# Kernel tuning notes

Measured on AMD Instinct MI355X. Metric: run time of the kernel, lower is better.

Reference implementation:

```python
import jax, jax.numpy as jnp
import numpy as np

D_MODEL = 1024
N_HEADS = 16
HEAD_DIM = D_MODEL // N_HEADS
NEG_INF = -1e9


def setup_inputs() -> dict:
    key = jax.random.key(0)
    ks = jax.random.split(key, 12)
    B, S = 2, 2048
    std = 1.0 / np.sqrt(D_MODEL)
    def lin(k):
        kw, kb = jax.random.split(k)
        W = jax.random.uniform(kw, (D_MODEL, D_MODEL), jnp.float32, -std, std)
        b = jax.random.uniform(kb, (D_MODEL,), jnp.float32, -std, std)
        return W, b
    Wq, bq = lin(ks[0])
    Wk, bk = lin(ks[1])
    Wv, bv = lin(ks[2])
    Wo, bo = lin(ks[3])
    Q = jax.random.normal(ks[4], (B, S, D_MODEL), jnp.float32)
    K = jax.random.normal(ks[5], (B, S, D_MODEL), jnp.float32)
    V = jax.random.normal(ks[6], (B, S, D_MODEL), jnp.float32)
    # causal attention mask: True means masked (disallowed)
    attn_mask = jnp.triu(jnp.ones((S, S), dtype=bool), k=1)
    padding_mask = jnp.zeros((B, S), dtype=bool)  # no padding
    return {"Q": Q, "K": K, "V": V, "attn_mask": attn_mask,
            "padding_mask": padding_mask,
            "Wq": Wq, "bq": bq, "Wk": Wk, "bk": bk,
            "Wv": Wv, "bv": bv, "Wo": Wo, "bo": bo}


def reference(Q, K, V, attn_mask, padding_mask, Wq, bq, Wk, bk, Wv, bv, Wo, bo):
    B, Sq, _ = Q.shape
    Sk = K.shape[1]
    # QKV projections, split into heads -> [B, H, S, Dh]
    def proj(x, W, b):
        y = x @ W.T + b
        return y.reshape(B, -1, N_HEADS, HEAD_DIM).transpose(0, 2, 1, 3)
    q = proj(Q, Wq, bq)
    k = proj(K, Wk, bk)
    v = proj(V, Wv, bv)
    # scaled dot-product attention (dropout is identity in eval mode)
    scores = jnp.einsum('bhqd,bhkd->bhqk', q, k) / jnp.sqrt(
        jnp.asarray(HEAD_DIM, q.dtype))
    mask = attn_mask[None, None, :, :] | padding_mask[:, None, None, :]
    scores = jnp.where(mask, NEG_INF, scores)
    attn = jax.nn.softmax(scores, axis=-1)
    x = jnp.einsum('bhqk,bhkd->bhqd', attn, v)
    x = x.transpose(0, 2, 1, 3).reshape(B, Sq, D_MODEL)
    return x @ Wo.T + bo
```

## Files before the change

kernel.cpp:

```cpp
#include <hip/hip_runtime.h>
#include <hip/hip_bf16.h>
#include <cstddef>
#include <cstdint>

#define S_LEN  2048
#define DMODEL 1024
#define NHEADS 16

typedef __attribute__((ext_vector_type(8))) short  short8;
typedef __attribute__((ext_vector_type(4))) short  s16x4;
typedef __attribute__((ext_vector_type(8))) __bf16 bf16x8;
typedef __attribute__((ext_vector_type(4))) float  f32x4;

__device__ __forceinline__ f32x4 MFMA(short8 a, short8 b, f32x4 c) {
    return __builtin_amdgcn_mfma_f32_16x16x32_bf16(
        __builtin_bit_cast(bf16x8, a), __builtin_bit_cast(bf16x8, b), c, 0, 0, 0);
}

__device__ __forceinline__ unsigned short f2bs(float f) {
    return __builtin_bit_cast(unsigned short, __float2bfloat16(f));
}
__device__ __forceinline__ float bs2f(unsigned short u) {
    unsigned int x = ((unsigned int)u) << 16;
    return __builtin_bit_cast(float, x);
}

__device__ __forceinline__ short8 cvt8(f32x4 a, f32x4 b) {
    short8 r;
#pragma unroll
    for (int i = 0; i < 4; ++i) {
        r[i]     = (short)f2bs(a[i]);
        r[4 + i] = (short)f2bs(b[i]);
    }
    return r;
}

__device__ __forceinline__ short8 scale8(short8 v) {
    short8 r;
#pragma unroll
    for (int i = 0; i < 8; ++i)
        r[i] = (short)f2bs(bs2f((unsigned short)v[i]) * 0.125f);
    return r;
}

__device__ __forceinline__ int xcd_swz(int bid, int nwg) {
    const int chunk = nwg >> 3;
    return (bid & 7) * chunk + (bid >> 3);
}

__device__ __forceinline__ void bar_sync() {
    asm volatile("s_waitcnt lgkmcnt(0)" ::: "memory");
    __builtin_amdgcn_sched_barrier(0);
    __builtin_amdgcn_s_barrier();
}

#define GLDS16(src, dst) __builtin_amdgcn_global_load_lds( \
    (__attribute__((address_space(1))) void*)(src),        \
    (__attribute__((address_space(3))) void*)(dst), 16, 0, 0)

struct FS { f32x4 v[2][2]; };

__global__ __launch_bounds__(256)
void wcvt(const float* __restrict__ Wq, const float* __restrict__ Wk,
          const float* __restrict__ Wv, unsigned short* __restrict__ wb)
{
    const int i = blockIdx.x * 256 + threadIdx.x;
    const float* src = (i < 131072) ? Wq : (i < 262144) ? Wk : Wv;
    const size_t j = (size_t)(i & 131071) * 8;
    const short8 v = cvt8(((const f32x4*)(src + j))[0], ((const f32x4*)(src + j))[1]);
    *(short8*)(wb + (size_t)i * 8) = v;
}

__global__ __launch_bounds__(256, 3)
void qkv_gemm(const float* __restrict__ Q, const float* __restrict__ K,
              const float* __restrict__ V,
              const unsigned short* __restrict__ wb,
              const float* __restrict__ bq, const float* __restrict__ bk,
              const float* __restrict__ bv,
              unsigned short* qh, unsigned short* kh, unsigned short* vh)
{
    __shared__ short a_lds[2][128 * 32];
    __shared__ short w_lds[2][128 * 32];

    const int swz = xcd_swz(blockIdx.x, 768);
    const int z   = swz >> 8;
    const int rem = swz & 255;
    const int m0  = (rem >> 3) * 128;
    const int n0  = (rem & 7) * 128;

    const float *A, *B_; unsigned short* O;
    if (z == 0)      { A = Q; B_ = bq; O = qh; }
    else if (z == 1) { A = K; B_ = bk; O = kh; }
    else             { A = V; B_ = bv; O = vh; }
    const unsigned short* W = wb + ((size_t)z << 20);

    const int t    = threadIdx.x;
    const int lane = t & 63;
    const int wid  = t >> 6;
    const int wr   = (wid >> 1) << 6;
    const int wc   = (wid & 1) << 6;
    const int fr   = lane & 15;
    const int ks   = lane >> 4;

    const int row0 = t >> 2,         sl0 = t & 3;
    const int row1 = (256 + t) >> 2, sl1 = (256 + t) & 3;
    const int ms0  = sl0 ^ ((row0 >> 1) & 3);
    const int ms1  = sl1 ^ ((row1 >> 1) & 3);

    const int g0 = wid * 2, g1 = g0 + 1;
    const int gsl   = lane & 3;
    const int grow0 = g0 * 16 + (lane >> 2);
    const int grow1 = g1 * 16 + (lane >> 2);
    const int ssl0  = gsl ^ ((grow0 >> 1) & 3);
    const int ssl1  = gsl ^ ((grow1 >> 1) & 3);

    auto load_R = [&](FS& S, int k0) {
        const float* p0 = A + (size_t)(m0 + row0) * DMODEL + k0 + sl0 * 8;
        S.v[0][0] = ((const f32x4*)p0)[0]; S.v[0][1] = ((const f32x4*)p0)[1];
        const float* p1 = A + (size_t)(m0 + row1) * DMODEL + k0 + sl1 * 8;
        S.v[1][0] = ((const f32x4*)p1)[0]; S.v[1][1] = ((const f32x4*)p1)[1];
    };
    auto store_R = [&](const FS& S, int buf) {
        *(short8*)&a_lds[buf][row0 * 32 + ms0 * 8] = cvt8(S.v[0][0], S.v[0][1]);
        *(short8*)&a_lds[buf][row1 * 32 + ms1 * 8] = cvt8(S.v[1][0], S.v[1][1]);
    };
    auto gload_G = [&](int k0, int buf) {
        GLDS16(W + (size_t)(n0 + grow0) * DMODEL + k0 + ssl0 * 8, &w_lds[buf][g0 * 512]);
        GLDS16(W + (size_t)(n0 + grow1) * DMODEL + k0 + ssl1 * 8, &w_lds[buf][g1 * 512]);
    };

    f32x4 acc[4][4] = {};
    auto compute = [&](int cur) {
        short8 af[4], bfr[4];
#pragma unroll
        for (int i = 0; i < 4; ++i) {
            const int ra = wr + i * 16 + fr;
            af[i]  = *(const short8*)&a_lds[cur][ra * 32 + ((ks ^ ((ra >> 1) & 3)) << 3)];
            const int rb = wc + i * 16 + fr;
            bfr[i] = *(const short8*)&w_lds[cur][rb * 32 + ((ks ^ ((rb >> 1) & 3)) << 3)];
        }
#pragma unroll
        for (int mi = 0; mi < 4; ++mi)
#pragma unroll
            for (int ni = 0; ni < 4; ++ni)
                acc[mi][ni] = MFMA(af[mi], bfr[ni], acc[mi][ni]);
    };

    FS SA, SB;
    gload_G(0, 0);
    load_R(SA, 0);
    store_R(SA, 0);
    load_R(SB, 32);
    bar_sync();

    for (int tt = 0; tt < 30; tt += 2) {
        gload_G((tt + 1) * 32, 1);
        load_R(SA, (tt + 2) * 32);
        compute(0);
        store_R(SB, 1);
        asm volatile("s_waitcnt vmcnt(4)" ::: "memory");
        bar_sync();
        gload_G((tt + 2) * 32, 0);
        load_R(SB, (tt + 3) * 32);
        compute(1);
        store_R(SA, 0);
        asm volatile("s_waitcnt vmcnt(4)" ::: "memory");
        bar_sync();
    }
    gload_G(31 * 32, 1);
    compute(0);
    store_R(SB, 1);
    asm volatile("s_waitcnt vmcnt(0)" ::: "memory");
    bar_sync();
    compute(1);

#pragma unroll
    for (int ni = 0; ni < 4; ++ni) {
        const int n    = n0 + wc + ni * 16 + fr;
        const float bv = B_[n];
#pragma unroll
        for (int mi = 0; mi < 4; ++mi) {
#pragma unroll
            for (int j = 0; j < 4; ++j) {
                const int m = m0 + wr + mi * 16 + ks * 4 + j;
                const int b = m >> 11, s = m & (S_LEN - 1);
                const int hh = n >> 6, dh = n & 63;
                O[((((size_t)b * NHEADS + hh) * S_LEN + s) << 6) + dh]
                    = f2bs(acc[mi][ni][j] + bv);
            }
        }
    }
}

__global__ __launch_bounds__(256, 3)
void out_gemm(const unsigned short* __restrict__ X, const float* __restrict__ Wo,
              const float* __restrict__ bo, float* __restrict__ out)
{
    __shared__ short a_lds[2][128 * 32];
    __shared__ short w_lds[2][128 * 32];
    const int swz = xcd_swz(blockIdx.x, 256);
    const int m0  = (swz >> 3) * 128;
    const int n0  = (swz & 7) * 128;

    const int t    = threadIdx.x;
    const int lane = t & 63;
    const int wid  = t >> 6;
    const int wr   = (wid >> 1) << 6;
    const int wc   = (wid & 1) << 6;
    const int fr   = lane & 15;
    const int ks   = lane >> 4;

    const int row0 = t >> 2,         sl0 = t & 3;
    const int row1 = (256 + t) >> 2, sl1 = (256 + t) & 3;
    const int ms0  = sl0 ^ ((row0 >> 1) & 3);
    const int ms1  = sl1 ^ ((row1 >> 1) & 3);

    short8 av_b[2];
    f32x4  wv_f[2][2];

    auto load_tile = [&](int k0) {
        av_b[0] = *(const short8*)(X + (size_t)(m0 + row0) * DMODEL + k0 + sl0 * 8);
        av_b[1] = *(const short8*)(X + (size_t)(m0 + row1) * DMODEL + k0 + sl1 * 8);
        const float* pw0 = Wo + (size_t)(n0 + row0) * DMODEL + k0 + sl0 * 8;
        wv_f[0][0] = ((const f32x4*)pw0)[0]; wv_f[0][1] = ((const f32x4*)pw0)[1];
        const float* pw1 = Wo + (size_t)(n0 + row1) * DMODEL + k0 + sl1 * 8;
        wv_f[1][0] = ((const f32x4*)pw1)[0]; wv_f[1][1] = ((const f32x4*)pw1)[1];
    };
    auto store_tile = [&](int buf) {
        *(short8*)&a_lds[buf][row0 * 32 + ms0 * 8] = av_b[0];
        *(short8*)&a_lds[buf][row1 * 32 + ms1 * 8] = av_b[1];
        *(short8*)&w_lds[buf][row0 * 32 + ms0 * 8] = cvt8(wv_f[0][0], wv_f[0][1]);
        *(short8*)&w_lds[buf][row1 * 32 + ms1 * 8] = cvt8(wv_f[1][0], wv_f[1][1]);
    };

    load_tile(0);
    store_tile(0);
    load_tile(32);
    __syncthreads();

    f32x4 acc[4][4] = {};

    for (int kidx = 0; kidx < 32; ++kidx) {
        const int cur = kidx & 1;
        short8 af[4], bfr[4];
#pragma unroll
        for (int i = 0; i < 4; ++i) {
            const int ra = wr + i * 16 + fr;
            af[i]  = *(const short8*)&a_lds[cur][ra * 32 + ((ks ^ ((ra >> 1) & 3)) << 3)];
            const int rb = wc + i * 16 + fr;
            bfr[i] = *(const short8*)&w_lds[cur][rb * 32 + ((ks ^ ((rb >> 1) & 3)) << 3)];
        }
#pragma unroll
        for (int mi = 0; mi < 4; ++mi)
#pragma unroll
            for (int ni = 0; ni < 4; ++ni)
                acc[mi][ni] = MFMA(af[mi], bfr[ni], acc[mi][ni]);

        if (kidx + 1 < 32) {
            store_tile(cur ^ 1);
            if (kidx + 2 < 32) load_tile((kidx + 2) * 32);
        }
        __syncthreads();
    }

#pragma unroll
    for (int ni = 0; ni < 4; ++ni) {
        const int n    = n0 + wc + ni * 16 + fr;
        const float bv = bo[n];
#pragma unroll
        for (int mi = 0; mi < 4; ++mi)
#pragma unroll
            for (int j = 0; j < 4; ++j) {
                const int m = m0 + wr + mi * 16 + ks * 4 + j;
                out[(size_t)m * DMODEL + n] = acc[mi][ni][j] + bv;
            }
    }
}

#define VSTR 72
#define PSTR 88

struct QState {
    short8 qf0, qf1;
    f32x4  oacc[4];
    float  m, l;
    int    qr0;
};

__device__ __forceinline__ void attn_tile(QState& st, const int k0,
                                          const short* k_lds, const short* v_lds,
                                          short* p_buf, const int fr, const int ks)
{
    const int myq = st.qr0 + fr;
    f32x4 sacc[4] = {};
    __builtin_amdgcn_s_setprio(1);
#pragma unroll
    for (int nk = 0; nk < 4; ++nk) {
        const int rb = nk * 16 + fr;
        short8 a0 = *(const short8*)&k_lds[rb * 64 + (((ks)     ^ (rb & 7)) << 3)];
        short8 a1 = *(const short8*)&k_lds[rb * 64 + (((4 + ks) ^ (rb & 7)) << 3)];
        sacc[nk] = MFMA(a0, st.qf0, sacc[nk]);
        sacc[nk] = MFMA(a1, st.qf1, sacc[nk]);
    }
    __builtin_amdgcn_s_setprio(0);

    float mx = -1e9f;
    if (k0 + 63 <= st.qr0) {
#pragma unroll
        for (int nk = 0; nk < 4; ++nk)
#pragma unroll
            for (int jj = 0; jj < 4; ++jj) mx = fmaxf(mx, sacc[nk][jj]);
    } else {
#pragma unroll
        for (int nk = 0; nk < 4; ++nk)
#pragma unroll
            for (int jj = 0; jj < 4; ++jj) {
                const int key = k0 + nk * 16 + ks * 4 + jj;
                float s = (key <= myq) ? sacc[nk][jj] : -1e9f;
                sacc[nk][jj] = s;
                mx = fmaxf(mx, s);
            }
    }
    mx = fmaxf(mx, __shfl_xor(mx, 16));
    mx = fmaxf(mx, __shfl_xor(mx, 32));
    if (!__all(mx <= st.m + 8.f)) {
        const float mnew = fmaxf(st.m, mx);
        const float corr = __expf(st.m - mnew);
        st.m = mnew;
        st.l *= corr;
#pragma unroll
        for (int nd = 0; nd < 4; ++nd)
#pragma unroll
            for (int jj = 0; jj < 4; ++jj) st.oacc[nd][jj] *= corr;
    }

    float rsum = 0.f;
#pragma unroll
    for (int nk = 0; nk < 4; ++nk) {
        s16x4 pw;
#pragma unroll
        for (int jj = 0; jj < 4; ++jj) {
            const float p = __expf(sacc[nk][jj] - st.m);
            rsum += p;
            pw[jj] = (short)f2bs(p);
        }
        *(s16x4*)&p_buf[fr * PSTR + nk * 16 + ks * 4] = pw;
    }
    rsum += __shfl_xor(rsum, 16);
    rsum += __shfl_xor(rsum, 32);
    st.l += rsum;
    asm volatile("" ::: "memory");

    __builtin_amdgcn_s_setprio(1);
#pragma unroll
    for (int sh = 0; sh < 2; ++sh) {
        short8 pa = *(const short8*)&p_buf[fr * PSTR + sh * 32 + ks * 8];
#pragma unroll
        for (int nd = 0; nd < 4; ++nd) {
            short8 vf = *(const short8*)&v_lds[(nd * 16 + fr) * VSTR + sh * 32 + ks * 8];
            st.oacc[nd] = MFMA(vf, pa, st.oacc[nd]);
        }
    }
    __builtin_amdgcn_s_setprio(0);
}

__global__ __launch_bounds__(256, 2)
void attn_kernel(const unsigned short* __restrict__ qh,
                 const unsigned short* __restrict__ kh,
                 const unsigned short* __restrict__ vh,
                 unsigned short* __restrict__ xh)
{
    __shared__ short k_lds[64 * 64];
    __shared__ short v_lds[64 * VSTR];
    __shared__ short p_lds[4][16 * PSTR];

    const int t    = threadIdx.x;
    const int lane = t & 63;
    const int wid  = t >> 6;
    const int fr   = lane & 15;
    const int ks   = lane >> 4;
    const int swz  = xcd_swz(blockIdx.x, 512);
    const int bh   = swz >> 4;
    const int xp   = swz & 15;
    const int qa0  = xp * 64;
    const int qb0  = (31 - xp) * 64;
    const int ntA  = xp + 1;
    const int ntB  = 32 - xp;

    const unsigned short* qb_ = qh + ((size_t)bh << 17);
    const unsigned short* kb  = kh + ((size_t)bh << 17);
    const unsigned short* vb  = vh + ((size_t)bh << 17);

    QState A, B;
    A.qr0 = qa0 + wid * 16;  B.qr0 = qb0 + wid * 16;
    A.qf0 = scale8(*(const short8*)&qb_[(A.qr0 + fr) * 64 + ks * 8]);
    A.qf1 = scale8(*(const short8*)&qb_[(A.qr0 + fr) * 64 + 32 + ks * 8]);
    B.qf0 = scale8(*(const short8*)&qb_[(B.qr0 + fr) * 64 + ks * 8]);
    B.qf1 = scale8(*(const short8*)&qb_[(B.qr0 + fr) * 64 + 32 + ks * 8]);
#pragma unroll
    for (int nd = 0; nd < 4; ++nd) { A.oacc[nd] = f32x4{}; B.oacc[nd] = f32x4{}; }
    A.m = B.m = -1e9f; A.l = B.l = 0.f;

    short8 kv[2], vv[2];
#pragma unroll
    for (int cc = 0; cc < 2; ++cc) {
        const int c   = cc * 256 + t;
        const int row = c >> 3;
        const int sl  = c & 7;
        kv[cc] = *(const short8*)(kb + (size_t)row * 64 + sl * 8);
        const int key = c & 63;
        const int d0  = (c >> 6) * 8;
        vv[cc] = *(const short8*)(vb + (size_t)key * 64 + d0);
    }

    for (int kt = 0; kt < ntB; ++kt) {
        const int k0 = kt * 64;
        __syncthreads();

#pragma unroll
        for (int cc = 0; cc < 2; ++cc) {
            const int c   = cc * 256 + t;
            const int row = c >> 3;
            const int ms  = (c & 7) ^ (row & 7);
            *(short8*)&k_lds[row * 64 + ms * 8] = kv[cc];
            const int key = c & 63;
            const int d0  = (c >> 6) * 8;
#pragma unroll
            for (int i = 0; i < 8; ++i)
                v_lds[(d0 + i) * VSTR + key] = vv[cc][i];
        }
        __syncthreads();

        if (kt + 1 < ntB) {
            const int k1 = k0 + 64;
#pragma unroll
            for (int cc = 0; cc < 2; ++cc) {
                const int c   = cc * 256 + t;
                const int row = c >> 3;
                const int sl  = c & 7;
                kv[cc] = *(const short8*)(kb + (size_t)(k1 + row) * 64 + sl * 8);
                const int key = c & 63;
                const int d0  = (c >> 6) * 8;
                vv[cc] = *(const short8*)(vb + (size_t)(k1 + key) * 64 + d0);
            }
        }

        attn_tile(B, k0, k_lds, v_lds, p_lds[wid], fr, ks);
        if (kt < ntA)
            attn_tile(A, k0, k_lds, v_lds, p_lds[wid], fr, ks);
    }

    const int b = bh >> 4, h = bh & 15;
#pragma unroll
    for (int which = 0; which < 2; ++which) {
        QState& st = which ? B : A;
        const float inv = 1.f / st.l;
        const size_t base = ((size_t)b * S_LEN + (st.qr0 + fr)) * DMODEL + h * 64;
#pragma unroll
        for (int nd = 0; nd < 4; ++nd)
#pragma unroll
            for (int jj = 0; jj < 4; ++jj)
                xh[base + nd * 16 + ks * 4 + jj] = f2bs(st.oacc[nd][jj] * inv);
    }
}

extern "C" void kernel_launch(void* const* d_in, const int* in_sizes, int n_in,
                              void* d_out, int out_size, void* d_ws, size_t ws_size,
                              hipStream_t stream)
{
    const float* Q  = (const float*)d_in[0];
    const float* K  = (const float*)d_in[1];
    const float* V  = (const float*)d_in[2];
    const float* Wq = (const float*)d_in[5];
    const float* bq = (const float*)d_in[6];
    const float* Wk = (const float*)d_in[7];
    const float* bk = (const float*)d_in[8];
    const float* Wv = (const float*)d_in[9];
    const float* bv = (const float*)d_in[10];
    const float* Wo = (const float*)d_in[11];
    const float* bo = (const float*)d_in[12];
    float* out = (float*)d_out;

    const size_t HSZ = (size_t)2 * S_LEN * DMODEL;
    unsigned short* qh = (unsigned short*)d_ws;
    unsigned short* kh = qh + HSZ;
    unsigned short* vh = kh + HSZ;
    unsigned short* xh = vh + HSZ;
    unsigned short* wb = xh;

    wcvt<<<1536, 256, 0, stream>>>(Wq, Wk, Wv, wb);
    qkv_gemm<<<768, 256, 0, stream>>>(Q, K, V, wb, bq, bk, bv, qh, kh, vh);
    attn_kernel<<<512, 256, 0, stream>>>(qh, kh, vh, xh);
    out_gemm<<<256, 256, 0, stream>>>(xh, Wo, bo, out);
}
```

Baseline: 109.1 us.

## Pre-convert activations and weights to bf16, use async LDS-load GEMMs

Adds a single conversion kernel that turns Q, K, V and all four weight matrices into bf16 in workspace. New QKV and output GEMM kernels then stream these bf16 operands straight into LDS with global_load_lds through a triple-buffered, swizzled pipeline. This is meant to remove the in-GEMM fp32 loads and conversions and halve the bytes each GEMM tile reads. The cost is an extra full pass over the activations plus a much larger workspace, and the old path stays as a fallback when the workspace is too small.

```diff
diff --git a/kernel.cpp b/kernel.cpp
--- a/kernel.cpp
+++ b/kernel.cpp
@@ -6,6 +6,8 @@
 #define S_LEN  2048
 #define DMODEL 1024
 #define NHEADS 16
+#define ELT    1048576
+#define HSZe   (4 * ELT)
 
 typedef __attribute__((ext_vector_type(8))) short  short8;
 typedef __attribute__((ext_vector_type(4))) short  s16x4;
@@ -59,6 +61,140 @@
     (__attribute__((address_space(3))) void*)(dst), 16, 0, 0)
 
 struct FS { f32x4 v[2][2]; };
+
+__global__ __launch_bounds__(256)
+void xcvt(const float* __restrict__ Q, const float* __restrict__ K,
+          const float* __restrict__ V,
+          const float* __restrict__ Wq, const float* __restrict__ Wk,
+          const float* __restrict__ Wv, const float* __restrict__ Wo,
+          unsigned short* __restrict__ dst)
+{
+    const int gid = blockIdx.x * 256 + threadIdx.x;
+    const size_t e0 = (size_t)gid * 8;
+    const int seg = (int)(e0 >> 20);
+    const float* src; size_t off;
+    if (seg < 4)        { src = Q;  off = e0; }
+    else if (seg < 8)   { src = K;  off = e0 - (size_t)4  * ELT; }
+    else if (seg < 12)  { src = V;  off = e0 - (size_t)8  * ELT; }
+    else if (seg == 12) { src = Wq; off = e0 - (size_t)12 * ELT; }
+    else if (seg == 13) { src = Wk; off = e0 - (size_t)13 * ELT; }
+    else if (seg == 14) { src = Wv; off = e0 - (size_t)14 * ELT; }
+    else                { src = Wo; off = e0 - (size_t)15 * ELT; }
+    *(short8*)(dst + e0) = cvt8(((const f32x4*)(src + off))[0],
+                                ((const f32x4*)(src + off))[1]);
+}
+
+template<bool SCATTER>
+__device__ __forceinline__ void gemm_gg(const unsigned short* __restrict__ A,
+                                        const unsigned short* __restrict__ W,
+                                        const float* __restrict__ bias,
+                                        void* __restrict__ outp,
+                                        int m0, int n0)
+{
+    __shared__ short a_lds[3][128 * 32];
+    __shared__ short w_lds[3][128 * 32];
+    const int t    = threadIdx.x;
+    const int lane = t & 63;
+    const int wid  = t >> 6;
+    const int wr   = (wid >> 1) << 6;
+    const int wc   = (wid & 1) << 6;
+    const int fr   = lane & 15;
+    const int ks   = lane >> 4;
+
+    const int g0 = wid * 2, g1 = g0 + 1;
+    const int gsl   = lane & 3;
+    const int grow0 = g0 * 16 + (lane >> 2);
+    const int grow1 = g1 * 16 + (lane >> 2);
+    const int ssl0  = gsl ^ ((grow0 >> 1) & 3);
+    const int ssl1  = gsl ^ ((grow1 >> 1) & 3);
+
+    auto gload = [&](int k0, int buf) {
+        GLDS16(A + (size_t)(m0 + grow0) * DMODEL + k0 + ssl0 * 8, &a_lds[buf][g0 * 512]);
+        GLDS16(A + (size_t)(m0 + grow1) * DMODEL + k0 + ssl1 * 8, &a_lds[buf][g1 * 512]);
+        GLDS16(W + (size_t)(n0 + grow0) * DMODEL + k0 + ssl0 * 8, &w_lds[buf][g0 * 512]);
+        GLDS16(W + (size_t)(n0 + grow1) * DMODEL + k0 + ssl1 * 8, &w_lds[buf][g1 * 512]);
+    };
+
+    f32x4 acc[4][4] = {};
+    auto compute = [&](int cur) {
+        short8 af[4], bfr[4];
+#pragma unroll
+        for (int i = 0; i < 4; ++i) {
+            const int ra = wr + i * 16 + fr;
+            af[i]  = *(const short8*)&a_lds[cur][ra * 32 + ((ks ^ ((ra >> 1) & 3)) << 3)];
+            const int rb = wc + i * 16 + fr;
+            bfr[i] = *(const short8*)&w_lds[cur][rb * 32 + ((ks ^ ((rb >> 1) & 3)) << 3)];
+        }
+#pragma unroll
+        for (int mi = 0; mi < 4; ++mi)
+#pragma unroll
+            for (int ni = 0; ni < 4; ++ni)
+                acc[mi][ni] = MFMA(af[mi], bfr[ni], acc[mi][ni]);
+    };
+
+    gload(0, 0);
+    gload(32, 1);
+
+    int cur = 0;
+    for (int tk = 0; tk < 32; ++tk) {
+        if (tk < 31) asm volatile("s_waitcnt vmcnt(4)" ::: "memory");
+        else         asm volatile("s_waitcnt vmcnt(0)" ::: "memory");
+        bar_sync();
+        if (tk + 2 < 32) {
+            int ib = cur + 2; if (ib >= 3) ib -= 3;
+            gload((tk + 2) * 32, ib);
+        }
+        compute(cur);
+        ++cur; if (cur == 3) cur = 0;
+    }
+
+#pragma unroll
+    for (int ni = 0; ni < 4; ++ni) {
+        const int n    = n0 + wc + ni * 16 + fr;
+        const float bv = bias[n];
+#pragma unroll
+        for (int mi = 0; mi < 4; ++mi) {
+#pragma unroll
+            for (int j = 0; j < 4; ++j) {
+                const int m = m0 + wr + mi * 16 + ks * 4 + j;
+                const float val = acc[mi][ni][j] + bv;
+                if constexpr (SCATTER) {
+                    const int b = m >> 11, s = m & (S_LEN - 1);
+                    const int hh = n >> 6, dh = n & 63;
+                    ((unsigned short*)outp)[((((size_t)b * NHEADS + hh) * S_LEN + s) << 6) + dh]
+                        = f2bs(val);
+                } else {
+                    ((float*)outp)[(size_t)m * DMODEL + n] = val;
+                }
+            }
+        }
+    }
+}
+
+__global__ __launch_bounds__(256, 3)
+void qkv_gemm_v2(const unsigned short* __restrict__ qx, const unsigned short* __restrict__ kx,
+                 const unsigned short* __restrict__ vx, const unsigned short* __restrict__ w3,
+                 const float* __restrict__ bq, const float* __restrict__ bk,
+                 const float* __restrict__ bv,
+                 unsigned short* qh, unsigned short* kh, unsigned short* vh)
+{
+    const int swz = xcd_swz(blockIdx.x, 768);
+    const int z   = swz >> 8;
+    const int rem = swz & 255;
+    const unsigned short *A; const float* B_; unsigned short* O;
+    if (z == 0)      { A = qx; B_ = bq; O = qh; }
+    else if (z == 1) { A = kx; B_ = bk; O = kh; }
+    else             { A = vx; B_ = bv; O = vh; }
+    gemm_gg<true>(A, w3 + ((size_t)z << 20), B_, O, (rem >> 3) * 128, (rem & 7) * 128);
+}
+
+__global__ __launch_bounds__(256, 3)
+void out_gemm_v2(const unsigned short* __restrict__ X, const unsigned short* __restrict__ wo,
+                 const float* __restrict__ bo, float* __restrict__ out)
+{
+    const int swz = xcd_swz(blockIdx.x, 256);
+    gemm_gg<false>(X, wo, bo, out, (swz >> 3) * 128, (swz & 7) * 128);
+}
 
 __global__ __launch_bounds__(256)
 void wcvt(const float* __restrict__ Wq, const float* __restrict__ Wk,
@@ -481,15 +617,33 @@
     const float* bo = (const float*)d_in[12];
     float* out = (float*)d_out;
 
-    const size_t HSZ = (size_t)2 * S_LEN * DMODEL;
-    unsigned short* qh = (unsigned short*)d_ws;
-    unsigned short* kh = qh + HSZ;
-    unsigned short* vh = kh + HSZ;
-    unsigned short* xh = vh + HSZ;
-    unsigned short* wb = xh;
-
-    wcvt<<<1536, 256, 0, stream>>>(Wq, Wk, Wv, wb);
-    qkv_gemm<<<768, 256, 0, stream>>>(Q, K, V, wb, bq, bk, bv, qh, kh, vh);
-    attn_kernel<<<512, 256, 0, stream>>>(qh, kh, vh, xh);
-    out_gemm<<<256, 256, 0, stream>>>(xh, Wo, bo, out);
-}
+    unsigned short* ws = (unsigned short*)d_ws;
+
+    if (ws_size >= (size_t)32 * ELT * 2) {
+        unsigned short* qx = ws;
+        unsigned short* kx = ws + (size_t)4  * ELT;
+        unsigned short* vx = ws + (size_t)8  * ELT;
+        unsigned short* w3 = ws + (size_t)12 * ELT;
+        unsigned short* wo = ws + (size_t)15 * ELT;
+        unsigned short* qh = ws + (size_t)16 * ELT;
+        unsigned short* kh = ws + (size_t)20 * ELT;
+        unsigned short* vh = ws + (size_t)24 * ELT;
+        unsigned short* xh = ws + (size_t)28 * ELT;
+
+        xcvt<<<8192, 256, 0, stream>>>(Q, K, V, Wq, Wk, Wv, Wo, ws);
+        qkv_gemm_v2<<<768, 256, 0, stream>>>(qx, kx, vx, w3, bq, bk, bv, qh, kh, vh);
+        attn_kernel<<<512, 256, 0, stream>>>(qh, kh, vh, xh);
+        out_gemm_v2<<<256, 256, 0, stream>>>(xh, wo, bo, out);
+    } else {
+        unsigned short* qh = ws;
+        unsigned short* kh = ws + (size_t)4  * ELT;
+        unsigned short* vh = ws + (size_t)8  * ELT;
+        unsigned short* xh = ws + (size_t)12 * ELT;
+        unsigned short* wb = xh;
+
+        wcvt<<<1536, 256, 0, stream>>>(Wq, Wk, Wv, wb);
+        qkv_gemm<<<768, 256, 0, stream>>>(Q, K, V, wb, bq, bk, bv, qh, kh, vh);
+        attn_kernel<<<512, 256, 0, stream>>>(qh, kh, vh, xh);
+        out_gemm<<<256, 256, 0, stream>>>(xh, Wo, bo, out);
+    }
+}
```

After: 118.4 us. 8.5% more time.
